# Kernel tuning notes

Hardware: AMD Instinct MI355X
Metric: run time of the kernel (lower is better)

## Reference

```python
import jax, jax.numpy as jnp
import numpy as np

N, C1, C2 = 1024, 384, 128
H, SQK, SV, PQK, PV, NCH = 12, 16, 16, 4, 8, 384
DIST_EPS = 1e-08
FEAT = H * SV + 3 * H * PV + H * PV + H * C2  # 2112


def setup_inputs() -> dict:
    key = jax.random.key(0)
    ks = jax.random.split(key, 20)
    inputs_1d = jax.random.normal(ks[0], (N, C1), jnp.float32)
    inputs_2d = jax.random.normal(ks[1], (N, N, C2), jnp.float32)
    mask = jnp.ones((N, 1), jnp.float32)
    # random valid rotations via QR
    rnd = jax.random.normal(ks[2], (N, 3, 3), jnp.float32)
    q, r = jnp.linalg.qr(rnd)
    rot = q * jnp.sign(jnp.diagonal(r, axis1=-2, axis2=-1))[:, None, :]
    trans = jax.random.normal(ks[3], (N, 3), jnp.float32) * 10.0
    s = lambda k, shape: jax.random.normal(k, shape, jnp.float32) * 0.02
    params = dict(
        raw_point_weights=jnp.full((H,), np.log(np.e - 1.0), jnp.float32),
        wq_point=s(ks[4], (C1, H, 3 * PQK)), bq_point=jnp.zeros((H, 3 * PQK), jnp.float32),
        wk_point=s(ks[5], (C1, H, 3 * PQK)), bk_point=jnp.zeros((H, 3 * PQK), jnp.float32),
        wv_point=s(ks[6], (C1, H, 3 * PV)), bv_point=jnp.zeros((H, 3 * PV), jnp.float32),
        wq_scalar=s(ks[7], (C1, H, SQK)),
        wk_scalar=s(ks[8], (C1, H, SQK)),
        wv_scalar=s(ks[9], (C1, H, SV)),
        w2d=s(ks[10], (C2, H)), b2d=jnp.zeros((H,), jnp.float32),
        wout=s(ks[11], (FEAT, NCH)), bout=jnp.zeros((NCH,), jnp.float32),
    )
    return dict(inputs_1d=inputs_1d, inputs_2d=inputs_2d, mask=mask, rot=rot, trans=trans, **params)


def _point_proj(x, w, b, rot, trans):
    # x: (N,C) -> global points (N,H,P,3)
    p = jnp.einsum('nc,chd->nhd', x, w, precision=jax.lax.Precision.HIGHEST) + b
    local = jnp.stack(jnp.split(p, 3, axis=-1), axis=-1)  # (N,H,P,3)
    return jnp.einsum('nij,nhpj->nhpi', rot, local) + trans[:, None, None, :]


def reference(inputs_1d, inputs_2d, mask, rot, trans,
              raw_point_weights, wq_point, bq_point, wk_point, bk_point,
              wv_point, bv_point, wq_scalar, wk_scalar, wv_scalar,
              w2d, b2d, wout, bout):
    point_var = max(PQK, 1) * 9.0 / 2
    point_weights = np.sqrt(1.0 / point_var) * jax.nn.softplus(raw_point_weights)  # (H,)

    q_point = _point_proj(inputs_1d, wq_point, bq_point, rot, trans)  # (N,H,Pqk,3)
    k_point = _point_proj(inputs_1d, wk_point, bk_point, rot, trans)
    # squared distances (q,k,h,p)
    diff = q_point[:, None] - k_point[None, :]
    dist2 = jnp.sum(diff * diff, axis=-1)
    attn_logits = -0.5 * jnp.sum(point_weights[None, None, :, None] * dist2, axis=-1)  # (q,k,h)

    scalar_w = np.sqrt(1.0 / max(SQK, 1))
    q_scalar = jnp.einsum('nc,chs->nhs', inputs_1d, wq_scalar) * scalar_w
    k_scalar = jnp.einsum('nc,chs->nhs', inputs_1d, wk_scalar)
    attn_logits += jnp.einsum('qhc,khc->qkh', q_scalar, k_scalar)

    attn_logits += jnp.einsum('qkc,ch->qkh', inputs_2d, w2d) + b2d

    mask_2d = mask * jnp.swapaxes(mask, -1, -2)  # (N,N)
    attn_logits = (attn_logits - 1e5 * (1.0 - mask_2d[..., None])) * np.sqrt(1.0 / 3)
    attn = jax.nn.softmax(attn_logits, axis=-2)  # softmax over k

    v_scalar = jnp.einsum('nc,chs->nhs', inputs_1d, wv_scalar)
    result_scalar = jnp.einsum('qkh,khc->qhc', attn, v_scalar).reshape(N, -1)

    v_point = _point_proj(inputs_1d, wv_point, bv_point, rot, trans)  # (N,H,Pv,3)
    res_pt_global = jnp.einsum('qkh,khpi->qhpi', attn, v_point)  # (q,H,Pv,3)
    # inverse rigid: R^T (p - t)
    res_pt_local = jnp.einsum('nji,nhpj->nhpi', rot, res_pt_global - trans[:, None, None, :])
    px = res_pt_local[..., 0].reshape(N, -1)
    py = res_pt_local[..., 1].reshape(N, -1)
    pz = res_pt_local[..., 2].reshape(N, -1)
    norm2 = jnp.sum(res_pt_local * res_pt_local, axis=-1)
    norms = jnp.sqrt(jnp.maximum(norm2, DIST_EPS * DIST_EPS)).reshape(N, -1)

    res_2d = jnp.einsum('ijh,ijc->ihc', attn, inputs_2d).reshape(N, -1)

    final = jnp.concatenate([result_scalar, px, py, pz, norms, res_2d], axis=-1)
    return final @ wout + bout
```

## Files before the change

### kernel.cpp

```cpp
#include <hip/hip_runtime.h>


#define NQ 1024
#define C1D 384
#define C2D 128
#define HH 12
#define FEATD 2112
#define NCHD 384

__global__ void k_prep(const float* __restrict__ raw, float* __restrict__ pwf) {
  int t = threadIdx.x;
  if (t < HH) {
    float x = raw[t];
    pwf[t] = 0.23570226039551584f * log1pf(expf(x));
  }
}

__global__ __launch_bounds__(256) void k_proj(
    const float* __restrict__ x1d, const float* __restrict__ rot, const float* __restrict__ trans,
    const float* __restrict__ wq_p, const float* __restrict__ bq_p,
    const float* __restrict__ wk_p, const float* __restrict__ bk_p,
    const float* __restrict__ wv_p, const float* __restrict__ bv_p,
    const float* __restrict__ wq_s, const float* __restrict__ wk_s, const float* __restrict__ wv_s,
    float* __restrict__ qs, float* __restrict__ ks_, float* __restrict__ vs,
    float* __restrict__ qp, float* __restrict__ kp, float* __restrict__ vp) {
  __shared__ float xs[8 * C1D];
  const int n0 = blockIdx.x * 8;
  const int t = threadIdx.x;
  for (int i = t; i < 8 * C1D; i += 256) xs[i] = x1d[(size_t)n0 * C1D + i];
  __syncthreads();
  const int u = blockIdx.y * 256 + t;
  if (u < 576) {
    const float* W; float* dst; float scale = 1.0f; int col;
    if (u < 192)      { W = wq_s; dst = qs;  col = u;       scale = 0.25f; }
    else if (u < 384) { W = wk_s; dst = ks_; col = u - 192; }
    else              { W = wv_s; dst = vs;  col = u - 384; }
    float acc[8];
#pragma unroll
    for (int r = 0; r < 8; ++r) acc[r] = 0.f;
    for (int c = 0; c < C1D; ++c) {
      float w = W[c * 192 + col];
#pragma unroll
      for (int r = 0; r < 8; ++r) acc[r] += xs[r * C1D + c] * w;
    }
    for (int r = 0; r < 8; ++r) dst[(size_t)(n0 + r) * 192 + col] = acc[r] * scale;
  } else {
    const float* W; const float* B; float* dst; int h, p, np_;
    if (u < 624)      { W = wq_p; B = bq_p; dst = qp; int v = u - 576; h = v / 4; p = v % 4; np_ = 4; }
    else if (u < 672) { W = wk_p; B = bk_p; dst = kp; int v = u - 624; h = v / 4; p = v % 4; np_ = 4; }
    else              { W = wv_p; B = bv_p; dst = vp; int v = u - 672; h = v / 8; p = v % 8; np_ = 8; }
    const int str = 36 * np_;
    const int c0 = h * 3 * np_ + p;
    float a0[8], a1[8], a2[8];
#pragma unroll
    for (int r = 0; r < 8; ++r) { a0[r] = 0.f; a1[r] = 0.f; a2[r] = 0.f; }
    for (int c = 0; c < C1D; ++c) {
      float w0 = W[c * str + c0];
      float w1 = W[c * str + c0 + np_];
      float w2 = W[c * str + c0 + 2 * np_];
#pragma unroll
      for (int r = 0; r < 8; ++r) {
        float x = xs[r * C1D + c];
        a0[r] += x * w0; a1[r] += x * w1; a2[r] += x * w2;
      }
    }
    const float b0 = B[c0], b1 = B[c0 + np_], b2 = B[c0 + 2 * np_];
    for (int r = 0; r < 8; ++r) {
      const int n = n0 + r;
      float l0 = a0[r] + b0, l1 = a1[r] + b1, l2 = a2[r] + b2;
      float R0 = rot[n * 9 + 0], R1 = rot[n * 9 + 1], R2 = rot[n * 9 + 2];
      float R3 = rot[n * 9 + 3], R4 = rot[n * 9 + 4], R5 = rot[n * 9 + 5];
      float R6 = rot[n * 9 + 6], R7 = rot[n * 9 + 7], R8 = rot[n * 9 + 8];
      float T0 = trans[n * 3 + 0], T1 = trans[n * 3 + 1], T2 = trans[n * 3 + 2];
      float g0 = R0 * l0 + R1 * l1 + R2 * l2 + T0;
      float g1 = R3 * l0 + R4 * l1 + R5 * l2 + T1;
      float g2 = R6 * l0 + R7 * l1 + R8 * l2 + T2;
      size_t o = (size_t)n * str + (size_t)(h * np_ + p) * 3;
      dst[o] = g0; dst[o + 1] = g1; dst[o + 2] = g2;
    }
  }
}

__global__ __launch_bounds__(512, 4) void k_attn(
    const float* __restrict__ x2d, const float* __restrict__ mask,
    const float* __restrict__ rot, const float* __restrict__ trans,
    const float* __restrict__ w2d, const float* __restrict__ b2d, const float* __restrict__ pwf,
    const float* __restrict__ qs, const float* __restrict__ ks_, const float* __restrict__ vs,
    const float* __restrict__ qp, const float* __restrict__ kp, const float* __restrict__ vp,
    float* __restrict__ feat) {
  __shared__ __attribute__((aligned(16))) float PT[HH * NQ];
  __shared__ __attribute__((aligned(16))) float qsl[192];
  __shared__ __attribute__((aligned(16))) float qpl[144];
  __shared__ float wred[8 * 12];
  __shared__ float mh[12], sinv[12];
  __shared__ float Gl[288];

  const int t = threadIdx.x;
  const int q = blockIdx.x;

  if (t < 192) qsl[t] = qs[(size_t)q * 192 + t];
  if (t >= 256 && t < 400) qpl[t - 256] = qp[(size_t)q * 144 + (t - 256)];

  float bh[12], pw[12];
#pragma unroll
  for (int h = 0; h < 12; ++h) { bh[h] = b2d[h]; pw[h] = pwf[h]; }
  const float mq = mask[q];
  __syncthreads();

  float pmax[12];
#pragma unroll
  for (int h = 0; h < 12; ++h) pmax[h] = -3.0e38f;

  for (int j = 0; j < 2; ++j) {
    const int k = t + j * 512;
    float acc[12];
#pragma unroll
    for (int h = 0; h < 12; ++h) acc[h] = bh[h];
    const float4* xr4 = (const float4*)(x2d + ((size_t)q * NQ + (size_t)k) * C2D);
#pragma unroll 4
    for (int g = 0; g < 32; ++g) {
      float4 xv = xr4[g];
      const float* wr = w2d + (g * 4) * 12;
#pragma unroll
      for (int h = 0; h < 12; ++h)
        acc[h] += xv.x * wr[h] + xv.y * wr[12 + h] + xv.z * wr[24 + h] + xv.w * wr[36 + h];
    }
    const float4* kr4 = (const float4*)(ks_ + (size_t)k * 192);
    const float4* qr4 = (const float4*)qsl;
#pragma unroll
    for (int h = 0; h < 12; ++h) {
      float d = 0.f;
#pragma unroll
      for (int jj = 0; jj < 4; ++jj) {
        float4 a = qr4[h * 4 + jj]; float4 b = kr4[h * 4 + jj];
        d += a.x * b.x + a.y * b.y + a.z * b.z + a.w * b.w;
      }
      acc[h] += d;
    }
    const float4* kp4 = (const float4*)(kp + (size_t)k * 144);
#pragma unroll
    for (int h = 0; h < 12; ++h) {
      float4 u0 = kp4[h * 3], u1 = kp4[h * 3 + 1], u2 = kp4[h * 3 + 2];
      const float* qb = &qpl[h * 12];
      float dx, dy, dz, d2 = 0.f;
      dx = qb[0] - u0.x; dy = qb[1]  - u0.y; dz = qb[2]  - u0.z; d2 += dx*dx + dy*dy + dz*dz;
      dx = qb[3] - u0.w; dy = qb[4]  - u1.x; dz = qb[5]  - u1.y; d2 += dx*dx + dy*dy + dz*dz;
      dx = qb[6] - u1.z; dy = qb[7]  - u1.w; dz = qb[8]  - u2.x; d2 += dx*dx + dy*dy + dz*dz;
      dx = qb[9] - u2.y; dy = qb[10] - u2.z; dz = qb[11] - u2.w; d2 += dx*dx + dy*dy + dz*dz;
      acc[h] -= 0.5f * pw[h] * d2;
    }
    const float mk = mask[k];
    const float mt = -100000.0f * (1.0f - mq * mk);
#pragma unroll
    for (int h = 0; h < 12; ++h) {
      float v = (acc[h] + mt) * 0.5773502691896258f;
      PT[h * NQ + k] = v;
      pmax[h] = fmaxf(pmax[h], v);
    }
  }

#pragma unroll
  for (int off = 32; off > 0; off >>= 1)
#pragma unroll
    for (int h = 0; h < 12; ++h) pmax[h] = fmaxf(pmax[h], __shfl_xor(pmax[h], off));
  const int wid = t >> 6, lane = t & 63;
  if (lane == 0)
#pragma unroll
    for (int h = 0; h < 12; ++h) wred[wid * 12 + h] = pmax[h];
  __syncthreads();
  if (t < 12) {
    float m = wred[t];
#pragma unroll
    for (int w = 1; w < 8; ++w) m = fmaxf(m, wred[w * 12 + t]);
    mh[t] = m;
  }
  __syncthreads();
  float psum[12];
#pragma unroll
  for (int h = 0; h < 12; ++h) psum[h] = 0.f;
  for (int j = 0; j < 2; ++j) {
    const int k = t + j * 512;
#pragma unroll
    for (int h = 0; h < 12; ++h) {
      float v = expf(PT[h * NQ + k] - mh[h]);
      PT[h * NQ + k] = v;
      psum[h] += v;
    }
  }
#pragma unroll
  for (int off = 32; off > 0; off >>= 1)
#pragma unroll
    for (int h = 0; h < 12; ++h) psum[h] += __shfl_xor(psum[h], off);
  if (lane == 0)
#pragma unroll
    for (int h = 0; h < 12; ++h) wred[wid * 12 + h] = psum[h];
  __syncthreads();
  if (t < 12) {
    float s = wred[t];
#pragma unroll
    for (int w = 1; w < 8; ++w) s += wred[w * 12 + t];
    sinv[t] = 1.0f / s;
  }
  __syncthreads();

  {
    const int c = t & 127;
    const int h0 = (t >> 7) * 3;
    float a0 = 0.f, a1 = 0.f, a2 = 0.f;
    const float* xc = x2d + (size_t)q * NQ * C2D + c;
    const float* Pa = &PT[(h0 + 0) * NQ];
    const float* Pb = &PT[(h0 + 1) * NQ];
    const float* Pc = &PT[(h0 + 2) * NQ];
    for (int k = 0; k < NQ; k += 8) {
      float x0 = xc[(size_t)(k + 0) * C2D], x1 = xc[(size_t)(k + 1) * C2D];
      float x2 = xc[(size_t)(k + 2) * C2D], x3 = xc[(size_t)(k + 3) * C2D];
      float x4 = xc[(size_t)(k + 4) * C2D], x5 = xc[(size_t)(k + 5) * C2D];
      float x6 = xc[(size_t)(k + 6) * C2D], x7 = xc[(size_t)(k + 7) * C2D];
      float4 pa0 = *(const float4*)&Pa[k], pa1 = *(const float4*)&Pa[k + 4];
      float4 pb0 = *(const float4*)&Pb[k], pb1 = *(const float4*)&Pb[k + 4];
      float4 pc0 = *(const float4*)&Pc[k], pc1 = *(const float4*)&Pc[k + 4];
      a0 += pa0.x * x0 + pa0.y * x1 + pa0.z * x2 + pa0.w * x3
          + pa1.x * x4 + pa1.y * x5 + pa1.z * x6 + pa1.w * x7;
      a1 += pb0.x * x0 + pb0.y * x1 + pb0.z * x2 + pb0.w * x3
          + pb1.x * x4 + pb1.y * x5 + pb1.z * x6 + pb1.w * x7;
      a2 += pc0.x * x0 + pc0.y * x1 + pc0.z * x2 + pc0.w * x3
          + pc1.x * x4 + pc1.y * x5 + pc1.z * x6 + pc1.w * x7;
    }
    float* fb = feat + (size_t)q * FEATD + 576 + c;
    fb[(size_t)(h0 + 0) * 128] = a0 * sinv[h0 + 0];
    fb[(size_t)(h0 + 1) * 128] = a1 * sinv[h0 + 1];
    fb[(size_t)(h0 + 2) * 128] = a2 * sinv[h0 + 2];
  }

  if (t < 480) {
    const int h = t / 40, r = t % 40;
    const float* src; int str, off;
    if (r < 16) { src = vs; str = 192; off = h * 16 + r; }
    else        { src = vp; str = 288; off = h * 24 + (r - 16); }
    const float* Ph = &PT[h * NQ];
    float acc = 0.f;
    for (int k = 0; k < NQ; k += 4) {
      acc += Ph[k]     * src[(size_t)(k)     * str + off]
           + Ph[k + 1] * src[(size_t)(k + 1) * str + off]
           + Ph[k + 2] * src[(size_t)(k + 2) * str + off]
           + Ph[k + 3] * src[(size_t)(k + 3) * str + off];
    }
    acc *= sinv[h];
    if (r < 16) feat[(size_t)q * FEATD + h * 16 + r] = acc;
    else Gl[h * 24 + (r - 16)] = acc;
  }
  __syncthreads();

  if (t < 96) {
    const int u = t;
    float R[9], T[3];
#pragma unroll
    for (int i = 0; i < 9; ++i) R[i] = rot[q * 9 + i];
#pragma unroll
    for (int i = 0; i < 3; ++i) T[i] = trans[q * 3 + i];
    float g0 = Gl[u * 3 + 0] - T[0];
    float g1 = Gl[u * 3 + 1] - T[1];
    float g2 = Gl[u * 3 + 2] - T[2];
    float l0 = R[0] * g0 + R[3] * g1 + R[6] * g2;
    float l1 = R[1] * g0 + R[4] * g1 + R[7] * g2;
    float l2 = R[2] * g0 + R[5] * g1 + R[8] * g2;
    float n2 = l0 * l0 + l1 * l1 + l2 * l2;
    float* fb = feat + (size_t)q * FEATD;
    fb[192 + u] = l0; fb[288 + u] = l1; fb[384 + u] = l2;
    fb[480 + u] = sqrtf(fmaxf(n2, 1e-16f));
  }
}

__global__ __launch_bounds__(256) void k_out(
    const float* __restrict__ feat, const float* __restrict__ wout,
    const float* __restrict__ bout, float* __restrict__ out) {
  __shared__ float A[32][33];
  __shared__ float B[32][33];
  const int t = threadIdx.x;
  const int row0 = blockIdx.x * 32, col0 = blockIdx.y * 32;
  const int r0 = t >> 4, c0 = t & 15;
  float acc[2][2] = {{0.f, 0.f}, {0.f, 0.f}};
  for (int k0 = 0; k0 < FEATD; k0 += 32) {
    for (int idx = t; idx < 1024; idx += 256) {
      int i = idx >> 5, j = idx & 31;
      A[i][j] = feat[(size_t)(row0 + i) * FEATD + k0 + j];
      B[i][j] = wout[(size_t)(k0 + i) * NCHD + col0 + j];
    }
    __syncthreads();
#pragma unroll 8
    for (int kk = 0; kk < 32; ++kk) {
      float a0 = A[r0][kk], a1 = A[r0 + 16][kk];
      float b0 = B[kk][c0], b1 = B[kk][c0 + 16];
      acc[0][0] += a0 * b0; acc[0][1] += a0 * b1;
      acc[1][0] += a1 * b0; acc[1][1] += a1 * b1;
    }
    __syncthreads();
  }
#pragma unroll
  for (int r = 0; r < 2; ++r)
#pragma unroll
    for (int c = 0; c < 2; ++c) {
      int rr = row0 + r0 + r * 16, cc = col0 + c0 + c * 16;
      out[(size_t)rr * NCHD + cc] = acc[r][c] + bout[cc];
    }
}

extern "C" void kernel_launch(void* const* d_in, const int* in_sizes, int n_in,
                              void* d_out, int out_size, void* d_ws, size_t ws_size,
                              hipStream_t stream) {
  const float* x1d   = (const float*)d_in[0];
  const float* x2d   = (const float*)d_in[1];
  const float* mask  = (const float*)d_in[2];
  const float* rot   = (const float*)d_in[3];
  const float* trans = (const float*)d_in[4];
  const float* raw   = (const float*)d_in[5];
  const float* wq_p  = (const float*)d_in[6];
  const float* bq_p  = (const float*)d_in[7];
  const float* wk_p  = (const float*)d_in[8];
  const float* bk_p  = (const float*)d_in[9];
  const float* wv_p  = (const float*)d_in[10];
  const float* bv_p  = (const float*)d_in[11];
  const float* wq_s  = (const float*)d_in[12];
  const float* wk_s  = (const float*)d_in[13];
  const float* wv_s  = (const float*)d_in[14];
  const float* w2d   = (const float*)d_in[15];
  const float* b2d   = (const float*)d_in[16];
  const float* wout  = (const float*)d_in[17];
  const float* bout  = (const float*)d_in[18];

  float* ws   = (float*)d_ws;
  float* qs   = ws;
  float* ks_  = qs  + 196608;
  float* vs   = ks_ + 196608;
  float* qp   = vs  + 196608;
  float* kp   = qp  + 147456;
  float* vp   = kp  + 147456;
  float* feat = vp  + 294912;
  float* pwf  = feat + 2162688;

  k_prep<<<dim3(1), 64, 0, stream>>>(raw, pwf);
  k_proj<<<dim3(128, 3), 256, 0, stream>>>(x1d, rot, trans, wq_p, bq_p, wk_p, bk_p,
                                           wv_p, bv_p, wq_s, wk_s, wv_s,
                                           qs, ks_, vs, qp, kp, vp);
  k_attn<<<dim3(1024), 512, 0, stream>>>(x2d, mask, rot, trans, w2d, b2d, pwf,
                                         qs, ks_, vs, qp, kp, vp, feat);
  k_out<<<dim3(32, 12), 256, 0, stream>>>(feat, wout, bout, (float*)d_out);
}
```

Before: 1.751 ms.

## Stream pair features in LDS chunks with online softmax in attention kernel

The attention kernel now processes keys in chunks of 128. Each chunk of inputs_2d is staged once in padded shared memory, with the next chunk prefetched into registers, and both the logit projection and the weighted pair-feature reduction read from that copy. Previously x2d was read from global memory twice per query. An online (flash-style) softmax with per-chunk rescaling replaces the full 12x1024 probability buffer, and logits are split as 3 heads per thread with a transposed w2d. The cost is many more block-wide barriers per chunk and serialized max/sum reductions.

Measured after the change: 5.595 ms. 3.19x slower.

```diff
diff --git a/kernel.cpp b/kernel.cpp
--- a/kernel.cpp
+++ b/kernel.cpp
@@ -7,12 +7,19 @@
 #define HH 12
 #define FEATD 2112
 #define NCHD 384
-
-__global__ void k_prep(const float* __restrict__ raw, float* __restrict__ pwf) {
+#define KC 128
+#define XPAD 132
+
+__global__ void k_prep(const float* __restrict__ raw, const float* __restrict__ w2d,
+                       float* __restrict__ pwf, float* __restrict__ w2dT) {
   int t = threadIdx.x;
   if (t < HH) {
     float x = raw[t];
     pwf[t] = 0.23570226039551584f * log1pf(expf(x));
+  }
+  for (int i = t; i < HH * C2D; i += 256) {
+    int h = i >> 7, c = i & 127;
+    w2dT[i] = w2d[c * HH + h];
   }
 }
 
@@ -84,190 +91,229 @@
 __global__ __launch_bounds__(512, 4) void k_attn(
     const float* __restrict__ x2d, const float* __restrict__ mask,
     const float* __restrict__ rot, const float* __restrict__ trans,
-    const float* __restrict__ w2d, const float* __restrict__ b2d, const float* __restrict__ pwf,
+    const float* __restrict__ w2dT, const float* __restrict__ b2d, const float* __restrict__ pwf,
     const float* __restrict__ qs, const float* __restrict__ ks_, const float* __restrict__ vs,
     const float* __restrict__ qp, const float* __restrict__ kp, const float* __restrict__ vp,
     float* __restrict__ feat) {
-  __shared__ __attribute__((aligned(16))) float PT[HH * NQ];
+  __shared__ __attribute__((aligned(16))) float Xs[KC * XPAD];
+  __shared__ __attribute__((aligned(16))) float P[HH * KC];
   __shared__ __attribute__((aligned(16))) float qsl[192];
   __shared__ __attribute__((aligned(16))) float qpl[144];
-  __shared__ float wred[8 * 12];
-  __shared__ float mh[12], sinv[12];
+  __shared__ float wred[96];
+  __shared__ float mh[12], al[12], sl[12];
   __shared__ float Gl[288];
 
   const int t = threadIdx.x;
+  const int lane = t & 63;
+  const int wav = t >> 6;
   const int q = blockIdx.x;
 
+  const int rL = (wav << 4) | (lane & 15);
+  const int h0 = 3 * (lane >> 4);
+  const int cR = t & 127;
+  const int hR = 3 * (t >> 7);
+  const int hV = t / 40;
+  const int rV = t % 40;
+  const float* vsrc; int vstr, voff;
+  if (rV < 16) { vsrc = vs; vstr = 192; voff = hV * 16 + rV; }
+  else         { vsrc = vp; vstr = 288; voff = hV * 24 + (rV - 16); }
+
   if (t < 192) qsl[t] = qs[(size_t)q * 192 + t];
-  if (t >= 256 && t < 400) qpl[t - 256] = qp[(size_t)q * 144 + (t - 256)];
-
-  float bh[12], pw[12];
-#pragma unroll
-  for (int h = 0; h < 12; ++h) { bh[h] = b2d[h]; pw[h] = pwf[h]; }
+  else if (t < 336) qpl[t - 192] = qp[(size_t)q * 144 + (t - 192)];
+  else if (t >= 448 && t < 460) { mh[t - 448] = -3.0e38f; sl[t - 448] = 0.f; }
+
+  const float bh0 = b2d[h0], bh1 = b2d[h0 + 1], bh2 = b2d[h0 + 2];
+  const float pw0 = pwf[h0], pw1 = pwf[h0 + 1], pw2 = pwf[h0 + 2];
   const float mq = mask[q];
-  __syncthreads();
-
-  float pmax[12];
-#pragma unroll
-  for (int h = 0; h < 12; ++h) pmax[h] = -3.0e38f;
-
-  for (int j = 0; j < 2; ++j) {
-    const int k = t + j * 512;
-    float acc[12];
-#pragma unroll
-    for (int h = 0; h < 12; ++h) acc[h] = bh[h];
-    const float4* xr4 = (const float4*)(x2d + ((size_t)q * NQ + (size_t)k) * C2D);
+
+  float a0 = 0.f, a1 = 0.f, a2 = 0.f;
+  float vacc = 0.f;
+
+  const float4* wa4 = (const float4*)(w2dT + (size_t)h0 * 128);
+  const float4* wb4 = (const float4*)(w2dT + (size_t)(h0 + 1) * 128);
+  const float4* wc4 = (const float4*)(w2dT + (size_t)(h0 + 2) * 128);
+  const float4* q4 = (const float4*)qsl;
+  const float4* gx = (const float4*)(x2d + (size_t)q * NQ * C2D);
+
+  float4 xbuf[8];
+#pragma unroll
+  for (int i = 0; i < 8; ++i) xbuf[i] = gx[t + i * 512];
+
+  for (int nc = 0; nc < 8; ++nc) {
+    const int k0 = nc * KC;
+    __syncthreads();
+#pragma unroll
+    for (int i = 0; i < 8; ++i) {
+      int idx = t + i * 512;
+      *(float4*)&Xs[(idx >> 5) * XPAD + (idx & 31) * 4] = xbuf[i];
+    }
+    __syncthreads();
+    if (nc < 7) {
+      const float4* gn = gx + (size_t)(nc + 1) * 4096;
+#pragma unroll
+      for (int i = 0; i < 8; ++i) xbuf[i] = gn[t + i * 512];
+    }
+
+    const int k = k0 + rL;
+    float A0 = bh0, A1 = bh1, A2 = bh2;
+    {
+      const float* xr = &Xs[rL * XPAD];
 #pragma unroll 4
-    for (int g = 0; g < 32; ++g) {
-      float4 xv = xr4[g];
-      const float* wr = w2d + (g * 4) * 12;
-#pragma unroll
-      for (int h = 0; h < 12; ++h)
-        acc[h] += xv.x * wr[h] + xv.y * wr[12 + h] + xv.z * wr[24 + h] + xv.w * wr[36 + h];
-    }
-    const float4* kr4 = (const float4*)(ks_ + (size_t)k * 192);
-    const float4* qr4 = (const float4*)qsl;
-#pragma unroll
-    for (int h = 0; h < 12; ++h) {
-      float d = 0.f;
+      for (int j = 0; j < 32; ++j) {
+        float4 x = *(const float4*)&xr[4 * j];
+        float4 u = wa4[j], v = wb4[j], w = wc4[j];
+        A0 += x.x * u.x + x.y * u.y + x.z * u.z + x.w * u.w;
+        A1 += x.x * v.x + x.y * v.y + x.z * v.z + x.w * v.w;
+        A2 += x.x * w.x + x.y * w.y + x.z * w.z + x.w * w.w;
+      }
+    }
+    {
+      const float4* kr4 = (const float4*)(ks_ + (size_t)k * 192);
 #pragma unroll
       for (int jj = 0; jj < 4; ++jj) {
-        float4 a = qr4[h * 4 + jj]; float4 b = kr4[h * 4 + jj];
-        d += a.x * b.x + a.y * b.y + a.z * b.z + a.w * b.w;
-      }
-      acc[h] += d;
-    }
-    const float4* kp4 = (const float4*)(kp + (size_t)k * 144);
-#pragma unroll
-    for (int h = 0; h < 12; ++h) {
-      float4 u0 = kp4[h * 3], u1 = kp4[h * 3 + 1], u2 = kp4[h * 3 + 2];
-      const float* qb = &qpl[h * 12];
-      float dx, dy, dz, d2 = 0.f;
+        float4 b0 = kr4[h0 * 4 + jj], b1 = kr4[(h0 + 1) * 4 + jj], b2 = kr4[(h0 + 2) * 4 + jj];
+        float4 qa = q4[h0 * 4 + jj],  qb = q4[(h0 + 1) * 4 + jj],  qc = q4[(h0 + 2) * 4 + jj];
+        A0 += qa.x * b0.x + qa.y * b0.y + qa.z * b0.z + qa.w * b0.w;
+        A1 += qb.x * b1.x + qb.y * b1.y + qb.z * b1.z + qb.w * b1.w;
+        A2 += qc.x * b2.x + qc.y * b2.y + qc.z * b2.z + qc.w * b2.w;
+      }
+    }
+    {
+      const float4* kp4 = (const float4*)(kp + (size_t)k * 144);
+      float4 u0, u1, u2; const float* qb; float dx, dy, dz, d2;
+      u0 = kp4[h0 * 3]; u1 = kp4[h0 * 3 + 1]; u2 = kp4[h0 * 3 + 2];
+      qb = &qpl[h0 * 12]; d2 = 0.f;
       dx = qb[0] - u0.x; dy = qb[1]  - u0.y; dz = qb[2]  - u0.z; d2 += dx*dx + dy*dy + dz*dz;
       dx = qb[3] - u0.w; dy = qb[4]  - u1.x; dz = qb[5]  - u1.y; d2 += dx*dx + dy*dy + dz*dz;
       dx = qb[6] - u1.z; dy = qb[7]  - u1.w; dz = qb[8]  - u2.x; d2 += dx*dx + dy*dy + dz*dz;
       dx = qb[9] - u2.y; dy = qb[10] - u2.z; dz = qb[11] - u2.w; d2 += dx*dx + dy*dy + dz*dz;
-      acc[h] -= 0.5f * pw[h] * d2;
-    }
-    const float mk = mask[k];
-    const float mt = -100000.0f * (1.0f - mq * mk);
-#pragma unroll
-    for (int h = 0; h < 12; ++h) {
-      float v = (acc[h] + mt) * 0.5773502691896258f;
-      PT[h * NQ + k] = v;
-      pmax[h] = fmaxf(pmax[h], v);
-    }
-  }
-
-#pragma unroll
-  for (int off = 32; off > 0; off >>= 1)
-#pragma unroll
-    for (int h = 0; h < 12; ++h) pmax[h] = fmaxf(pmax[h], __shfl_xor(pmax[h], off));
-  const int wid = t >> 6, lane = t & 63;
-  if (lane == 0)
-#pragma unroll
-    for (int h = 0; h < 12; ++h) wred[wid * 12 + h] = pmax[h];
+      A0 -= 0.5f * pw0 * d2;
+      u0 = kp4[(h0 + 1) * 3]; u1 = kp4[(h0 + 1) * 3 + 1]; u2 = kp4[(h0 + 1) * 3 + 2];
+      qb = &qpl[(h0 + 1) * 12]; d2 = 0.f;
+      dx = qb[0] - u0.x; dy = qb[1]  - u0.y; dz = qb[2]  - u0.z; d2 += dx*dx + dy*dy + dz*dz;
+      dx = qb[3] - u0.w; dy = qb[4]  - u1.x; dz = qb[5]  - u1.y; d2 += dx*dx + dy*dy + dz*dz;
+      dx = qb[6] - u1.z; dy = qb[7]  - u1.w; dz = qb[8]  - u2.x; d2 += dx*dx + dy*dy + dz*dz;
+      dx = qb[9] - u2.y; dy = qb[10] - u2.z; dz = qb[11] - u2.w; d2 += dx*dx + dy*dy + dz*dz;
+      A1 -= 0.5f * pw1 * d2;
+      u0 = kp4[(h0 + 2) * 3]; u1 = kp4[(h0 + 2) * 3 + 1]; u2 = kp4[(h0 + 2) * 3 + 2];
+      qb = &qpl[(h0 + 2) * 12]; d2 = 0.f;
+      dx = qb[0] - u0.x; dy = qb[1]  - u0.y; dz = qb[2]  - u0.z; d2 += dx*dx + dy*dy + dz*dz;
+      dx = qb[3] - u0.w; dy = qb[4]  - u1.x; dz = qb[5]  - u1.y; d2 += dx*dx + dy*dy + dz*dz;
+      dx = qb[6] - u1.z; dy = qb[7]  - u1.w; dz = qb[8]  - u2.x; d2 += dx*dx + dy*dy + dz*dz;
+      dx = qb[9] - u2.y; dy = qb[10] - u2.z; dz = qb[11] - u2.w; d2 += dx*dx + dy*dy + dz*dz;
+      A2 -= 0.5f * pw2 * d2;
+    }
+    {
+      const float mk = mask[k];
+      const float mt = -100000.0f * (1.0f - mq * mk);
+      A0 = (A0 + mt) * 0.5773502691896258f;
+      A1 = (A1 + mt) * 0.5773502691896258f;
+      A2 = (A2 + mt) * 0.5773502691896258f;
+    }
+    {
+      float m0 = A0, m1 = A1, m2 = A2;
+#pragma unroll
+      for (int off = 1; off < 16; off <<= 1) {
+        m0 = fmaxf(m0, __shfl_xor(m0, off));
+        m1 = fmaxf(m1, __shfl_xor(m1, off));
+        m2 = fmaxf(m2, __shfl_xor(m2, off));
+      }
+      if ((lane & 15) == 0) {
+        wred[wav * 12 + h0] = m0; wred[wav * 12 + h0 + 1] = m1; wred[wav * 12 + h0 + 2] = m2;
+      }
+    }
+    __syncthreads();
+    if (t < 12) {
+      float mc = wred[t];
+#pragma unroll
+      for (int w = 1; w < 8; ++w) mc = fmaxf(mc, wred[w * 12 + t]);
+      float mo = mh[t], mn = fmaxf(mo, mc);
+      al[t] = expf(mo - mn);
+      mh[t] = mn;
+    }
+    __syncthreads();
+    {
+      float e0 = expf(A0 - mh[h0]);
+      float e1 = expf(A1 - mh[h0 + 1]);
+      float e2 = expf(A2 - mh[h0 + 2]);
+      P[h0 * KC + rL] = e0; P[(h0 + 1) * KC + rL] = e1; P[(h0 + 2) * KC + rL] = e2;
+#pragma unroll
+      for (int off = 1; off < 16; off <<= 1) {
+        e0 += __shfl_xor(e0, off); e1 += __shfl_xor(e1, off); e2 += __shfl_xor(e2, off);
+      }
+      if ((lane & 15) == 0) {
+        wred[wav * 12 + h0] = e0; wred[wav * 12 + h0 + 1] = e1; wred[wav * 12 + h0 + 2] = e2;
+      }
+    }
+    __syncthreads();
+    if (t < 12) {
+      float s = 0.f;
+#pragma unroll
+      for (int w = 0; w < 8; ++w) s += wred[w * 12 + t];
+      sl[t] = sl[t] * al[t] + s;
+    }
+    {
+      a0 *= al[hR]; a1 *= al[hR + 1]; a2 *= al[hR + 2];
+      const float* xc = &Xs[cR];
+      const float* Pa = &P[hR * KC];
+      const float* Pb = &P[(hR + 1) * KC];
+      const float* Pc = &P[(hR + 2) * KC];
+      for (int kk = 0; kk < KC; kk += 4) {
+        float4 p0 = *(const float4*)&Pa[kk];
+        float4 p1 = *(const float4*)&Pb[kk];
+        float4 p2 = *(const float4*)&Pc[kk];
+        float x0 = xc[kk * XPAD],       x1 = xc[(kk + 1) * XPAD];
+        float x2 = xc[(kk + 2) * XPAD], x3 = xc[(kk + 3) * XPAD];
+        a0 += p0.x * x0 + p0.y * x1 + p0.z * x2 + p0.w * x3;
+        a1 += p1.x * x0 + p1.y * x1 + p1.z * x2 + p1.w * x3;
+        a2 += p2.x * x0 + p2.y * x1 + p2.z * x2 + p2.w * x3;
+      }
+    }
+    if (t < 480) {
+      vacc *= al[hV];
+      const float* Ph = &P[hV * KC];
+      const float* src = vsrc + (size_t)k0 * vstr + voff;
+#pragma unroll 4
+      for (int kk = 0; kk < KC; kk += 4) {
+        float4 p = *(const float4*)&Ph[kk];
+        vacc += p.x * src[(size_t)kk * vstr]
+              + p.y * src[(size_t)(kk + 1) * vstr]
+              + p.z * src[(size_t)(kk + 2) * vstr]
+              + p.w * src[(size_t)(kk + 3) * vstr];
+      }
+    }
+  }
   __syncthreads();
-  if (t < 12) {
-    float m = wred[t];
-#pragma unroll
-    for (int w = 1; w < 8; ++w) m = fmaxf(m, wred[w * 12 + t]);
-    mh[t] = m;
-  }
+  if (t < 12) mh[t] = 1.0f / sl[t];
   __syncthreads();
-  float psum[12];
-#pragma unroll
-  for (int h = 0; h < 12; ++h) psum[h] = 0.f;
-  for (int j = 0; j < 2; ++j) {
-    const int k = t + j * 512;
-#pragma unroll
-    for (int h = 0; h < 12; ++h) {
-      float v = expf(PT[h * NQ + k] - mh[h]);
-      PT[h * NQ + k] = v;
-      psum[h] += v;
-    }
-  }
-#pragma unroll
-  for (int off = 32; off > 0; off >>= 1)
-#pragma unroll
-    for (int h = 0; h < 12; ++h) psum[h] += __shfl_xor(psum[h], off);
-  if (lane == 0)
-#pragma unroll
-    for (int h = 0; h < 12; ++h) wred[wid * 12 + h] = psum[h];
+  {
+    float* fb = feat + (size_t)q * FEATD + 576 + cR;
+    fb[(size_t)hR * 128]       = a0 * mh[hR];
+    fb[(size_t)(hR + 1) * 128] = a1 * mh[hR + 1];
+    fb[(size_t)(hR + 2) * 128] = a2 * mh[hR + 2];
+  }
+  if (t < 480) {
+    float v = vacc * mh[hV];
+    if (rV < 16) feat[(size_t)q * FEATD + hV * 16 + rV] = v;
+    else Gl[hV * 24 + (rV - 16)] = v;
+  }
   __syncthreads();
-  if (t < 12) {
-    float s = wred[t];
-#pragma unroll
-    for (int w = 1; w < 8; ++w) s += wred[w * 12 + t];
-    sinv[t] = 1.0f / s;
-  }
-  __syncthreads();
-
-  {
-    const int c = t & 127;
-    const int h0 = (t >> 7) * 3;
-    float a0 = 0.f, a1 = 0.f, a2 = 0.f;
-    const float* xc = x2d + (size_t)q * NQ * C2D + c;
-    const float* Pa = &PT[(h0 + 0) * NQ];
-    const float* Pb = &PT[(h0 + 1) * NQ];
-    const float* Pc = &PT[(h0 + 2) * NQ];
-    for (int k = 0; k < NQ; k += 8) {
-      float x0 = xc[(size_t)(k + 0) * C2D], x1 = xc[(size_t)(k + 1) * C2D];
-      float x2 = xc[(size_t)(k + 2) * C2D], x3 = xc[(size_t)(k + 3) * C2D];
-      float x4 = xc[(size_t)(k + 4) * C2D], x5 = xc[(size_t)(k + 5) * C2D];
-      float x6 = xc[(size_t)(k + 6) * C2D], x7 = xc[(size_t)(k + 7) * C2D];
-      float4 pa0 = *(const float4*)&Pa[k], pa1 = *(const float4*)&Pa[k + 4];
-      float4 pb0 = *(const float4*)&Pb[k], pb1 = *(const float4*)&Pb[k + 4];
-      float4 pc0 = *(const float4*)&Pc[k], pc1 = *(const float4*)&Pc[k + 4];
-      a0 += pa0.x * x0 + pa0.y * x1 + pa0.z * x2 + pa0.w * x3
-          + pa1.x * x4 + pa1.y * x5 + pa1.z * x6 + pa1.w * x7;
-      a1 += pb0.x * x0 + pb0.y * x1 + pb0.z * x2 + pb0.w * x3
-          + pb1.x * x4 + pb1.y * x5 + pb1.z * x6 + pb1.w * x7;
-      a2 += pc0.x * x0 + pc0.y * x1 + pc0.z * x2 + pc0.w * x3
-          + pc1.x * x4 + pc1.y * x5 + pc1.z * x6 + pc1.w * x7;
-    }
-    float* fb = feat + (size_t)q * FEATD + 576 + c;
-    fb[(size_t)(h0 + 0) * 128] = a0 * sinv[h0 + 0];
-    fb[(size_t)(h0 + 1) * 128] = a1 * sinv[h0 + 1];
-    fb[(size_t)(h0 + 2) * 128] = a2 * sinv[h0 + 2];
-  }
-
-  if (t < 480) {
-    const int h = t / 40, r = t % 40;
-    const float* src; int str, off;
-    if (r < 16) { src = vs; str = 192; off = h * 16 + r; }
-    else        { src = vp; str = 288; off = h * 24 + (r - 16); }
-    const float* Ph = &PT[h * NQ];
-    float acc = 0.f;
-    for (int k = 0; k < NQ; k += 4) {
-      acc += Ph[k]     * src[(size_t)(k)     * str + off]
-           + Ph[k + 1] * src[(size_t)(k + 1) * str + off]
-           + Ph[k + 2] * src[(size_t)(k + 2) * str + off]
-           + Ph[k + 3] * src[(size_t)(k + 3) * str + off];
-    }
-    acc *= sinv[h];
-    if (r < 16) feat[(size_t)q * FEATD + h * 16 + r] = acc;
-    else Gl[h * 24 + (r - 16)] = acc;
-  }
-  __syncthreads();
-
   if (t < 96) {
-    const int u = t;
     float R[9], T[3];
 #pragma unroll
     for (int i = 0; i < 9; ++i) R[i] = rot[q * 9 + i];
 #pragma unroll
     for (int i = 0; i < 3; ++i) T[i] = trans[q * 3 + i];
-    float g0 = Gl[u * 3 + 0] - T[0];
-    float g1 = Gl[u * 3 + 1] - T[1];
-    float g2 = Gl[u * 3 + 2] - T[2];
+    float g0 = Gl[t * 3 + 0] - T[0];
+    float g1 = Gl[t * 3 + 1] - T[1];
+    float g2 = Gl[t * 3 + 2] - T[2];
     float l0 = R[0] * g0 + R[3] * g1 + R[6] * g2;
     float l1 = R[1] * g0 + R[4] * g1 + R[7] * g2;
     float l2 = R[2] * g0 + R[5] * g1 + R[8] * g2;
     float n2 = l0 * l0 + l1 * l1 + l2 * l2;
     float* fb = feat + (size_t)q * FEATD;
-    fb[192 + u] = l0; fb[288 + u] = l1; fb[384 + u] = l2;
-    fb[480 + u] = sqrtf(fmaxf(n2, 1e-16f));
+    fb[192 + t] = l0; fb[288 + t] = l1; fb[384 + t] = l2;
+    fb[480 + t] = sqrtf(fmaxf(n2, 1e-16f));
   }
 }
 
@@ -337,12 +383,13 @@
   float* vp   = kp  + 147456;
   float* feat = vp  + 294912;
   float* pwf  = feat + 2162688;
-
-  k_prep<<<dim3(1), 64, 0, stream>>>(raw, pwf);
+  float* w2dT = pwf + 12;
+
+  k_prep<<<dim3(1), 256, 0, stream>>>(raw, w2d, pwf, w2dT);
   k_proj<<<dim3(128, 3), 256, 0, stream>>>(x1d, rot, trans, wq_p, bq_p, wk_p, bk_p,
                                            wv_p, bv_p, wq_s, wk_s, wv_s,
                                            qs, ks_, vs, qp, kp, vp);
-  k_attn<<<dim3(1024), 512, 0, stream>>>(x2d, mask, rot, trans, w2d, b2d, pwf,
+  k_attn<<<dim3(1024), 512, 0, stream>>>(x2d, mask, rot, trans, w2dT, b2d, pwf,
                                          qs, ks_, vs, qp, kp, vp, feat);
   k_out<<<dim3(32, 12), 256, 0, stream>>>(feat, wout, bout, (float*)d_out);
 }
```

## Transpose value projections and compute scalar/point aggregation with wave-level reductions

Applied to the files above, without the earlier changes.

The projection kernel now writes scalar and point values in a transposed (feature-major) layout. The attention kernel then computes each of the 480 value outputs with a whole 64-lane wavefront, using float4 loads over keys and a shuffle reduction. Before, each output ran on a single thread reading strided global memory. This targets uncoalesced, serial per-thread loops in the value aggregation stage, at the cost of scattered strided writes in the projection kernel.

Result: no change. 1.752 ms (+0.0%).

```diff
diff --git a/kernel.cpp b/kernel.cpp
--- a/kernel.cpp
+++ b/kernel.cpp
@@ -22,8 +22,8 @@
     const float* __restrict__ wk_p, const float* __restrict__ bk_p,
     const float* __restrict__ wv_p, const float* __restrict__ bv_p,
     const float* __restrict__ wq_s, const float* __restrict__ wk_s, const float* __restrict__ wv_s,
-    float* __restrict__ qs, float* __restrict__ ks_, float* __restrict__ vs,
-    float* __restrict__ qp, float* __restrict__ kp, float* __restrict__ vp) {
+    float* __restrict__ qs, float* __restrict__ ks_, float* __restrict__ vsT,
+    float* __restrict__ qp, float* __restrict__ kp, float* __restrict__ vpT) {
   __shared__ float xs[8 * C1D];
   const int n0 = blockIdx.x * 8;
   const int t = threadIdx.x;
@@ -31,10 +31,10 @@
   __syncthreads();
   const int u = blockIdx.y * 256 + t;
   if (u < 576) {
-    const float* W; float* dst; float scale = 1.0f; int col;
-    if (u < 192)      { W = wq_s; dst = qs;  col = u;       scale = 0.25f; }
-    else if (u < 384) { W = wk_s; dst = ks_; col = u - 192; }
-    else              { W = wv_s; dst = vs;  col = u - 384; }
+    const float* W; float scale = 1.0f; int col;
+    if (u < 192)      { W = wq_s; col = u;       scale = 0.25f; }
+    else if (u < 384) { W = wk_s; col = u - 192; }
+    else              { W = wv_s; col = u - 384; }
     float acc[8];
 #pragma unroll
     for (int r = 0; r < 8; ++r) acc[r] = 0.f;
@@ -43,12 +43,19 @@
 #pragma unroll
       for (int r = 0; r < 8; ++r) acc[r] += xs[r * C1D + c] * w;
     }
-    for (int r = 0; r < 8; ++r) dst[(size_t)(n0 + r) * 192 + col] = acc[r] * scale;
+    if (u < 192) {
+      for (int r = 0; r < 8; ++r) qs[(size_t)(n0 + r) * 192 + col] = acc[r] * scale;
+    } else if (u < 384) {
+      for (int r = 0; r < 8; ++r) ks_[(size_t)(n0 + r) * 192 + col] = acc[r];
+    } else {
+      for (int r = 0; r < 8; ++r) vsT[(size_t)col * NQ + n0 + r] = acc[r];
+    }
   } else {
-    const float* W; const float* B; float* dst; int h, p, np_;
+    const float* W; const float* B; int h, p, np_; bool isV = false;
+    float* dst;
     if (u < 624)      { W = wq_p; B = bq_p; dst = qp; int v = u - 576; h = v / 4; p = v % 4; np_ = 4; }
     else if (u < 672) { W = wk_p; B = bk_p; dst = kp; int v = u - 624; h = v / 4; p = v % 4; np_ = 4; }
-    else              { W = wv_p; B = bv_p; dst = vp; int v = u - 672; h = v / 8; p = v % 8; np_ = 8; }
+    else              { W = wv_p; B = bv_p; dst = vpT; int v = u - 672; h = v / 8; p = v % 8; np_ = 8; isV = true; }
     const int str = 36 * np_;
     const int c0 = h * 3 * np_ + p;
     float a0[8], a1[8], a2[8];
@@ -75,8 +82,13 @@
       float g0 = R0 * l0 + R1 * l1 + R2 * l2 + T0;
       float g1 = R3 * l0 + R4 * l1 + R5 * l2 + T1;
       float g2 = R6 * l0 + R7 * l1 + R8 * l2 + T2;
-      size_t o = (size_t)n * str + (size_t)(h * np_ + p) * 3;
-      dst[o] = g0; dst[o + 1] = g1; dst[o + 2] = g2;
+      if (isV) {
+        size_t e = (size_t)(h * 8 + p) * 3;
+        dst[e * NQ + n] = g0; dst[(e + 1) * NQ + n] = g1; dst[(e + 2) * NQ + n] = g2;
+      } else {
+        size_t o = (size_t)n * 144 + (size_t)(h * 4 + p) * 3;
+        dst[o] = g0; dst[o + 1] = g1; dst[o + 2] = g2;
+      }
     }
   }
 }
@@ -85,8 +97,8 @@
     const float* __restrict__ x2d, const float* __restrict__ mask,
     const float* __restrict__ rot, const float* __restrict__ trans,
     const float* __restrict__ w2d, const float* __restrict__ b2d, const float* __restrict__ pwf,
-    const float* __restrict__ qs, const float* __restrict__ ks_, const float* __restrict__ vs,
-    const float* __restrict__ qp, const float* __restrict__ kp, const float* __restrict__ vp,
+    const float* __restrict__ qs, const float* __restrict__ ks_, const float* __restrict__ vsT,
+    const float* __restrict__ qp, const float* __restrict__ kp, const float* __restrict__ vpT,
     float* __restrict__ feat) {
   __shared__ __attribute__((aligned(16))) float PT[HH * NQ];
   __shared__ __attribute__((aligned(16))) float qsl[192];
@@ -232,22 +244,26 @@
     fb[(size_t)(h0 + 2) * 128] = a2 * sinv[h0 + 2];
   }
 
-  if (t < 480) {
-    const int h = t / 40, r = t % 40;
-    const float* src; int str, off;
-    if (r < 16) { src = vs; str = 192; off = h * 16 + r; }
-    else        { src = vp; str = 288; off = h * 24 + (r - 16); }
-    const float* Ph = &PT[h * NQ];
+  for (int o = wid; o < 480; o += 8) {
+    const int h = o / 40, r = o % 40;
+    const float* srcT = (r < 16) ? (vsT + (size_t)(h * 16 + r) * NQ)
+                                 : (vpT + (size_t)(h * 24 + (r - 16)) * NQ);
+    const float4* s4 = (const float4*)srcT;
+    const float4* p4 = (const float4*)&PT[h * NQ];
     float acc = 0.f;
-    for (int k = 0; k < NQ; k += 4) {
-      acc += Ph[k]     * src[(size_t)(k)     * str + off]
-           + Ph[k + 1] * src[(size_t)(k + 1) * str + off]
-           + Ph[k + 2] * src[(size_t)(k + 2) * str + off]
-           + Ph[k + 3] * src[(size_t)(k + 3) * str + off];
-    }
-    acc *= sinv[h];
-    if (r < 16) feat[(size_t)q * FEATD + h * 16 + r] = acc;
-    else Gl[h * 24 + (r - 16)] = acc;
+#pragma unroll
+    for (int pass = 0; pass < 4; ++pass) {
+      float4 v = s4[pass * 64 + lane];
+      float4 p = p4[pass * 64 + lane];
+      acc += v.x * p.x + v.y * p.y + v.z * p.z + v.w * p.w;
+    }
+#pragma unroll
+    for (int off = 32; off > 0; off >>= 1) acc += __shfl_xor(acc, off);
+    if (lane == 0) {
+      float val = acc * sinv[h];
+      if (r < 16) feat[(size_t)q * FEATD + h * 16 + r] = val;
+      else Gl[h * 24 + (r - 16)] = val;
+    }
   }
   __syncthreads();
 
@@ -331,18 +347,18 @@
   float* ws   = (float*)d_ws;
   float* qs   = ws;
   float* ks_  = qs  + 196608;
-  float* vs   = ks_ + 196608;
-  float* qp   = vs  + 196608;
+  float* vsT  = ks_ + 196608;
+  float* qp   = vsT + 196608;
   float* kp   = qp  + 147456;
-  float* vp   = kp  + 147456;
-  float* feat = vp  + 294912;
+  float* vpT  = kp  + 147456;
+  float* feat = vpT + 294912;
   float* pwf  = feat + 2162688;
 
   k_prep<<<dim3(1), 64, 0, stream>>>(raw, pwf);
   k_proj<<<dim3(128, 3), 256, 0, stream>>>(x1d, rot, trans, wq_p, bq_p, wk_p, bk_p,
                                            wv_p, bv_p, wq_s, wk_s, wv_s,
-                                           qs, ks_, vs, qp, kp, vp);
+                                           qs, ks_, vsT, qp, kp, vpT);
   k_attn<<<dim3(1024), 512, 0, stream>>>(x2d, mask, rot, trans, w2d, b2d, pwf,
-                                         qs, ks_, vs, qp, kp, vp, feat);
+                                         qs, ks_, vsT, qp, kp, vpT, feat);
   k_out<<<dim3(32, 12), 256, 0, stream>>>(feat, wout, bout, (float*)d_out);
 }
```
